# Performance work log

Measured on AMD Instinct MI355X. Metric: run time of the kernel, lower is better.

## Reference

```python
import jax, jax.numpy as jnp
import numpy as np

# ---- config constants (must match init_kwargs) ----
B, S, D, H, HD = 2, 2048, 512, 8, 64
N_BLK, L_BLK = 64, 32          # block_size, block_len (S = N_BLK*L_BLK)
R, RM = 8, 4                   # router_size, group_router_mul_factor
LN, GN, GE, GT = 8, 4, 16, 2   # moe layers, groups, group experts, topk per token
DR, DG = 128, 128
FFH = 1024
THETA = 10000.0
EPS = 1e-6

_INV_FREQ = (1.0 / THETA) ** (np.arange(0, HD, 2, dtype=np.float32) / HD)


def rmsnorm(x, w):
    return x * jax.lax.rsqrt(jnp.mean(x * x, axis=-1, keepdims=True) + EPS) * w


def rope(x):
    # x: (b, h, s, hd); y1 = x1*cos + x2*sin, y2 = -x1*sin + x2*cos (as in RotaryEmb)
    s = x.shape[2]
    freqs = jnp.outer(jnp.arange(s, dtype=jnp.float32), jnp.asarray(_INV_FREQ))[None, None]
    cos, sin = jnp.cos(freqs), jnp.sin(freqs)
    x1, x2 = jnp.split(x, 2, axis=-1)
    return jnp.concatenate([x1 * cos + x2 * sin, -x1 * sin + x2 * cos], axis=-1)


def layer(x, mask, qkv_w, o_w, up_w, down_w, n1, n2):
    b, s, d = x.shape
    xn = rmsnorm(x, n1)
    q, k, v = jnp.split(xn @ qkv_w, 3, axis=-1)
    sh = lambda t: t.reshape(b, s, H, HD).transpose(0, 2, 1, 3)  # b h s hd
    q, k, v = rope(sh(q)), rope(sh(k)), sh(v)
    scores = jnp.einsum('bhqa,bhka->bhqk', q, k) / np.sqrt(HD).astype(np.float32)
    if mask is not None:
        scores = jnp.where(mask[:, None], scores, -jnp.inf)
    p = jax.nn.softmax(scores, axis=-1)
    o = jnp.einsum('bhqk,bhka->bhqa', p, v).transpose(0, 2, 1, 3).reshape(b, s, d)
    x = x + o @ o_w
    xn2 = rmsnorm(x, n2)
    h1, h2 = jnp.split(xn2 @ up_w, 2, axis=-1)
    return x + (jax.nn.silu(h1) * h2) @ down_w


def _l2n(t, axis):
    return t / jnp.maximum(jnp.linalg.norm(t, axis=axis, keepdims=True), 1e-12)


def forward(x, doc, router_token, out_w, keys_router, keys_gate,
            enc_qkv, enc_o, enc_up, enc_down, enc_n1, enc_n2,
            rtr_qkv, rtr_o, rtr_up, rtr_down, rtr_n1, rtr_n2):
    # ---- AuxEncoder: block-causal AND same-document mask (global_attn branch) ----
    qb = jnp.arange(S) // N_BLK
    causal = qb[:, None] >= qb[None, :]                       # (S, S)
    mask = causal[None] & (doc[:, :, None] == doc[:, None, :])  # (B, S, S)
    for i in range(enc_qkv.shape[0]):
        x = layer(x, mask, enc_qkv[i], enc_o[i], enc_up[i], enc_down[i], enc_n1[i], enc_n2[i])

    # ---- AuxRouter: split into blocks, append router tokens, full attention ----
    xr = x.reshape(B * L_BLK, N_BLK, D)
    rt = jnp.broadcast_to(router_token, (B * L_BLK, R, D))
    xr = jnp.concatenate([xr, rt], axis=1)                    # (B*L, N+R, D)
    for i in range(rtr_qkv.shape[0]):
        xr = layer(xr, None, rtr_qkv[i], rtr_o[i], rtr_up[i], rtr_down[i], rtr_n1[i], rtr_n2[i])
    out = xr[:, N_BLK:] @ out_w                               # (B*L, R, DR+DG)
    xro, xgo = out[..., :DR], out[..., DR:]

    def expand(t, dd):
        # repeat '(b l) r d -> (r rm) b l d', roll(1, dim=2), flatten(1,2)
        t = t.reshape(B, L_BLK, R, dd).transpose(2, 0, 1, 3)  # (R, B, L, d)
        t = jnp.repeat(t, RM, axis=0)                          # (R*RM, B, L, d)
        t = jnp.roll(t, 1, axis=2)
        return t.reshape(R * RM, B * L_BLK, dd)

    xrr = _l2n(expand(xro, DR), -1)
    xgg = _l2n(expand(xgo, DG), -1)
    kr = _l2n(keys_router, 1)
    kg = _l2n(keys_gate, 1)
    rl = jnp.einsum('gbd,gde->gbe', xrr, kr)                  # (LN*GN, B*L, GE)
    gl = jnp.einsum('gbd,gde->gbe', xgg, kg)
    _, idx = jax.lax.top_k(rl, GT)                            # (LN*GN, B*L, GT)
    rv = jnp.take_along_axis(rl, idx, axis=-1)
    gv = jnp.take_along_axis(gl, idx, axis=-1)
    return jnp.stack([rv, gv], axis=0)                        # (2, 32, 64, 2)


def setup_inputs() -> dict:
    key = jax.random.key(0)
    ks = jax.random.split(key, 20)
    w = lambda k, shp: 0.02 * jax.random.normal(k, shp, dtype=jnp.float32)
    return {
        'x': jax.random.normal(ks[0], (B, S, D), dtype=jnp.float32),
        'doc': jnp.sort(jax.random.randint(ks[1], (B, S), 0, 4), axis=-1),
        'router_token': jax.random.normal(ks[2], (1, R, D), dtype=jnp.float32),
        'out_w': w(ks[3], (D, DR + DG)),
        'keys_router': jax.random.normal(ks[4], (LN * GN, DR, GE), dtype=jnp.float32),
        'keys_gate': jax.random.normal(ks[5], (LN * GN, DG, GE), dtype=jnp.float32),
        'enc_qkv': w(ks[6], (4, D, 3 * D)),
        'enc_o': w(ks[7], (4, D, D)),
        'enc_up': w(ks[8], (4, D, 2 * FFH)),
        'enc_down': w(ks[9], (4, FFH, D)),
        'enc_n1': jnp.ones((4, D), dtype=jnp.float32),
        'enc_n2': jnp.ones((4, D), dtype=jnp.float32),
        'rtr_qkv': w(ks[10], (2, D, 3 * D)),
        'rtr_o': w(ks[11], (2, D, D)),
        'rtr_up': w(ks[12], (2, D, 2 * FFH)),
        'rtr_down': w(ks[13], (2, FFH, D)),
        'rtr_n1': jnp.ones((2, D), dtype=jnp.float32),
        'rtr_n2': jnp.ones((2, D), dtype=jnp.float32),
    }


def reference(x, doc, router_token, out_w, keys_router, keys_gate,
              enc_qkv, enc_o, enc_up, enc_down, enc_n1, enc_n2,
              rtr_qkv, rtr_o, rtr_up, rtr_down, rtr_n1, rtr_n2):
    return forward(x, doc, router_token, out_w, keys_router, keys_gate,
                   enc_qkv, enc_o, enc_up, enc_down, enc_n1, enc_n2,
                   rtr_qkv, rtr_o, rtr_up, rtr_down, rtr_n1, rtr_n2)
```

## Files before the change

### kernel.cpp

```cpp
#include <hip/hip_runtime.h>
#include <hip/hip_bf16.h>
#include <cstdint>


typedef __attribute__((ext_vector_type(8))) short short8;
typedef __attribute__((ext_vector_type(4))) float f32x4;
typedef unsigned short ushort_t;

__device__ __forceinline__ float bf2f(unsigned short u) {
    return __uint_as_float(((unsigned)u) << 16);
}
__device__ __forceinline__ unsigned short f2bf(float f) {
    unsigned u = __float_as_uint(f);
    unsigned r = 0x7FFFu + ((u >> 16) & 1u);
    return (unsigned short)((u + r) >> 16);
}
__device__ __forceinline__ float wave_sum64(float v) {
#pragma unroll
    for (int o = 32; o; o >>= 1) v += __shfl_xor(v, o);
    return v;
}
__device__ __forceinline__ void load_lds16(const ushort_t* g, ushort_t* l) {
    __builtin_amdgcn_global_load_lds(
        (const __attribute__((address_space(1))) unsigned int*)g,
        (__attribute__((address_space(3))) unsigned int*)l, 16, 0, 0);
}

#define MFMA16(a, b, c) __builtin_amdgcn_mfma_f32_16x16x32_bf16(a, b, c, 0, 0, 0)
#define BARRIER_RAW() do { asm volatile("" ::: "memory"); \
    __builtin_amdgcn_s_barrier(); asm volatile("" ::: "memory"); } while (0)

__global__ void copy_in_kernel(const float* __restrict__ src,
                               float* __restrict__ dst, int n) {
    int i = blockIdx.x * 256 + threadIdx.x;
    if (i < n) dst[i] = src[i];
}

__global__ __launch_bounds__(256) void wsplit_kernel(const float* __restrict__ W,
        unsigned short* __restrict__ WH, unsigned short* __restrict__ WL,
        int K, int N) {
    __shared__ float tile[32][33];
    int bn = blockIdx.x * 32, bk = blockIdx.y * 32;
    int tx = threadIdx.x & 31, ty = threadIdx.x >> 5;
#pragma unroll
    for (int i = 0; i < 4; ++i)
        tile[ty + 8 * i][tx] = W[(size_t)(bk + ty + 8 * i) * N + bn + tx];
    __syncthreads();
#pragma unroll
    for (int i = 0; i < 4; ++i) {
        int n = bn + ty + 8 * i, k = bk + tx;
        float x = tile[tx][ty + 8 * i];
        unsigned short h = f2bf(x);
        unsigned short lo = f2bf(x - bf2f(h));
        WH[(size_t)n * K + k] = h;
        WL[(size_t)n * K + k] = lo;
    }
}

__global__ __launch_bounds__(256) void rmsnorm_kernel(const float* __restrict__ X,
        const float* __restrict__ W, ushort_t* __restrict__ XNH,
        ushort_t* __restrict__ XNL) {
    int t = blockIdx.x, tid = threadIdx.x;
    const float* xr = X + (size_t)t * 512;
    float v0 = xr[tid], v1 = xr[tid + 256];
    float ss = wave_sum64(v0 * v0 + v1 * v1);
    __shared__ float red[4];
    if ((tid & 63) == 0) red[tid >> 6] = ss;
    __syncthreads();
    float tot = red[0] + red[1] + red[2] + red[3];
    float scale = rsqrtf(tot * (1.0f / 512.0f) + 1e-6f);
    float a0 = v0 * scale * W[tid];
    float a1 = v1 * scale * W[tid + 256];
    unsigned short h0 = f2bf(a0), h1 = f2bf(a1);
    size_t base = (size_t)t * 512;
    XNH[base + tid]       = h0;
    XNL[base + tid]       = f2bf(a0 - bf2f(h0));
    XNH[base + tid + 256] = h1;
    XNL[base + tid + 256] = f2bf(a1 - bf2f(h1));
}

template <int BM>
__global__ __launch_bounds__(256) void gemm3(
        const ushort_t* __restrict__ AH, const ushort_t* __restrict__ AL,
        const ushort_t* __restrict__ BH, const ushort_t* __restrict__ BL,
        const float* __restrict__ Res, float* __restrict__ C,
        int M, int N, int K) {
    constexpr int MI   = BM / 32;
    constexpr int ROWS = 2 * BM + 256;
    constexpr int LPW  = ROWS / 64;
    constexpr int SS   = ROWS * 32;
    __shared__ __align__(16) ushort_t S[3][ROWS][32];
    int tid = threadIdx.x;
    int n0 = blockIdx.x * 128, m0 = blockIdx.y * BM;
    int wid = tid >> 6, lane = tid & 63;
    int wm = (wid >> 1) * (BM / 2), wn = (wid & 1) * 64;
    int col = lane & 15, quad = lane >> 4;

    const ushort_t* gsrc[LPW];
    int ldof[LPW];
#pragma unroll
    for (int j = 0; j < LPW; ++j) {
        int e = wid * LPW + j;
        int srow = e * 16 + (lane >> 2);
        const ushort_t* gp; int rin;
        if (srow < BM)                { gp = AH + (size_t)m0 * K; rin = srow; }
        else if (srow < 2 * BM)       { gp = AL + (size_t)m0 * K; rin = srow - BM; }
        else if (srow < 2 * BM + 128) { gp = BH + (size_t)n0 * K; rin = srow - 2 * BM; }
        else                          { gp = BL + (size_t)n0 * K; rin = srow - 2 * BM - 128; }
        gsrc[j] = gp + (size_t)rin * K + ((lane & 3) ^ ((lane >> 3) & 3)) * 8;
        ldof[j] = e * 512;
    }
    ushort_t* sbase = &S[0][0][0];
    auto STAGE = [&](int set, int kc) {
        ushort_t* sb = sbase + set * SS;
#pragma unroll
        for (int j = 0; j < LPW; ++j)
            load_lds16(gsrc[j] + kc * 32, sb + ldof[j]);
    };
    auto WAITK = [&]() {
        if constexpr (BM == 64) asm volatile("s_waitcnt vmcnt(6)" ::: "memory");
        else                    asm volatile("s_waitcnt vmcnt(8)" ::: "memory");
    };

    int chrd = (quad ^ ((col >> 1) & 3)) * 8;
    f32x4 acc[MI][4] = {};
    int nk = K >> 5;
    STAGE(0, 0);
    if (nk > 1) { STAGE(1, 1); WAITK(); }
    else        { asm volatile("s_waitcnt vmcnt(0)" ::: "memory"); }
    BARRIER_RAW();
    int sc = 0, sn = 1, sp = 2;
#pragma unroll 1
    for (int kc = 0; kc < nk; ++kc) {
        if (kc + 2 < nk) STAGE(sp, kc + 2);
        const ushort_t* sb = sbase + sc * SS;
        short8 afh[MI], afl[MI], bfh[4], bfl[4];
#pragma unroll
        for (int i = 0; i < MI; ++i) {
            afh[i] = *(const short8*)(sb + (size_t)(wm + i * 16 + col) * 32 + chrd);
            afl[i] = *(const short8*)(sb + (size_t)(BM + wm + i * 16 + col) * 32 + chrd);
        }
#pragma unroll
        for (int i = 0; i < 4; ++i) {
            bfh[i] = *(const short8*)(sb + (size_t)(2 * BM + wn + i * 16 + col) * 32 + chrd);
            bfl[i] = *(const short8*)(sb + (size_t)(2 * BM + 128 + wn + i * 16 + col) * 32 + chrd);
        }
#pragma unroll
        for (int mi = 0; mi < MI; ++mi)
#pragma unroll
            for (int ni = 0; ni < 4; ++ni) {
                f32x4 c = acc[mi][ni];
                c = MFMA16(afh[mi], bfh[ni], c);
                c = MFMA16(afh[mi], bfl[ni], c);
                c = MFMA16(afl[mi], bfh[ni], c);
                acc[mi][ni] = c;
            }
        if (kc + 1 < nk) {
            if (kc + 2 < nk) WAITK();
            else asm volatile("s_waitcnt vmcnt(0)" ::: "memory");
            BARRIER_RAW();
        }
        int t = sc; sc = sn; sn = sp; sp = t;
    }
#pragma unroll
    for (int mi = 0; mi < MI; ++mi)
#pragma unroll
        for (int ni = 0; ni < 4; ++ni)
#pragma unroll
            for (int r = 0; r < 4; ++r) {
                int row = m0 + wm + mi * 16 + quad * 4 + r;
                int ccol = n0 + wn + ni * 16 + col;
                size_t o = (size_t)row * N + ccol;
                float v = acc[mi][ni][r];
                if (Res) v += Res[o];
                C[o] = v;
            }
}

__global__ void rope_pack_kernel(const float* __restrict__ QKV,
        float* __restrict__ Q, ushort_t* __restrict__ KH,
        ushort_t* __restrict__ KL, int Sg, int total) {
    int idx = blockIdx.x * 256 + threadIdx.x;
    if (idx >= total) return;
    int i = idx & 31;
    int h = (idx >> 5) & 7;
    int t = idx >> 8;
    int g = t / Sg; int s = t - g * Sg;
    const float* row = QKV + (size_t)t * 1536;
    float inv = powf(10000.0f, -(float)(2 * i) / 64.0f);
    float sn, cs;
    sincosf((float)s * inv, &sn, &cs);
    size_t ob = ((size_t)(g * 8 + h) * Sg + s) * 64 + i;
    int c = h * 64 + i;
    float q1 = row[c], q2 = row[c + 32];
    Q[ob]      = q1 * cs + q2 * sn;
    Q[ob + 32] = q2 * cs - q1 * sn;
    float k1 = row[512 + c], k2 = row[512 + c + 32];
    float ka = k1 * cs + k2 * sn;
    float kb = k2 * cs - k1 * sn;
    unsigned short ha = f2bf(ka), hb = f2bf(kb);
    KH[ob]      = ha;  KL[ob]      = f2bf(ka - bf2f(ha));
    KH[ob + 32] = hb;  KL[ob + 32] = f2bf(kb - bf2f(hb));
}

__global__ __launch_bounds__(256) void vtrans_kernel(const float* __restrict__ QKV,
        ushort_t* __restrict__ VTH, ushort_t* __restrict__ VTL, int Sg) {
    __shared__ float tile[64][65];
    int chunk = blockIdx.x, gh = blockIdx.y;
    int g = gh >> 3, h = gh & 7;
    int tid = threadIdx.x;
    int sr = tid >> 2, dc = (tid & 3) * 16;
    int s = chunk * 64 + sr;
    if (s < Sg) {
        const float* src = QKV + ((size_t)g * Sg + s) * 1536 + 1024 + h * 64 + dc;
#pragma unroll
        for (int j = 0; j < 4; ++j) {
            float4 v = *(const float4*)(src + 4 * j);
            tile[sr][dc + 4 * j]     = v.x;
            tile[sr][dc + 4 * j + 1] = v.y;
            tile[sr][dc + 4 * j + 2] = v.z;
            tile[sr][dc + 4 * j + 3] = v.w;
        }
    } else {
#pragma unroll
        for (int j = 0; j < 16; ++j) tile[sr][dc + j] = 0.f;
    }
    __syncthreads();
    int dr = tid >> 2, sc = (tid & 3) * 16;
    short8 hv[2], lv[2];
#pragma unroll
    for (int half = 0; half < 2; ++half)
#pragma unroll
        for (int j = 0; j < 8; ++j) {
            float v = tile[sc + half * 8 + j][dr];
            unsigned short hb = f2bf(v);
            hv[half][j] = (short)hb;
            lv[half][j] = (short)f2bf(v - bf2f(hb));
        }
    int scol = chunk * 64 + sc;
    size_t ob = ((size_t)gh * 64 + dr) * Sg + scol;
    if (scol + 16 <= Sg) {
        *(short8*)(VTH + ob)     = hv[0];
        *(short8*)(VTH + ob + 8) = hv[1];
        *(short8*)(VTL + ob)     = lv[0];
        *(short8*)(VTL + ob + 8) = lv[1];
    } else {
#pragma unroll
        for (int j = 0; j < 16; ++j)
            if (scol + j < Sg) {
                VTH[ob + j] = (ushort_t)((j < 8) ? hv[0][j] : hv[1][j - 8]);
                VTL[ob + j] = (ushort_t)((j < 8) ? lv[0][j] : lv[1][j - 8]);
            }
    }
}

template <bool MASKED>
__global__ __launch_bounds__(256, 3) void attn3_kernel(const float* __restrict__ Q,
        const ushort_t* __restrict__ KHg, const ushort_t* __restrict__ KLg,
        const ushort_t* __restrict__ VTHg, const ushort_t* __restrict__ VTLg,
        const int* __restrict__ doc, ushort_t* __restrict__ AOH,
        ushort_t* __restrict__ AOL, int Sg) {
    __shared__ __align__(16) ushort_t Khs[64][64], Kls[64][64];
    __shared__ __align__(16) ushort_t Vts[64][64], Vtl[64][64];
    __shared__ __align__(16) ushort_t Ph[4][16][72], Pl[4][16][72];
    __shared__ int dock[64];
    int qb = (int)(gridDim.x - 1 - blockIdx.x);
    int gh = blockIdx.y, g = gh >> 3;
    int tid = threadIdx.x, wid = tid >> 6, lane = tid & 63;
    int col = lane & 15, quad = lane >> 4;

    int rL = lane >> 3, cSw = (lane & 7) ^ rL;
    const ushort_t* kb;
    const ushort_t* vb;
    ushort_t* lb;
    if (wid == 0)      { kb = KHg + (size_t)gh * Sg * 64 + cSw * 8;  vb = nullptr; lb = &Khs[0][0]; }
    else if (wid == 1) { kb = KLg + (size_t)gh * Sg * 64 + cSw * 8;  vb = nullptr; lb = &Kls[0][0]; }
    else if (wid == 2) { vb = VTHg + ((size_t)gh * 64 + rL) * Sg;    kb = nullptr; lb = &Vts[0][0]; }
    else               { vb = VTLg + ((size_t)gh * 64 + rL) * Sg;    kb = nullptr; lb = &Vtl[0][0]; }
    int sw0 = ((0 + quad) ^ (col & 7)) * 8;
    int sw1 = ((4 + quad) ^ (col & 7)) * 8;

    short8 qa[2][2];
    {
        int qrow = qb * 64 + wid * 16 + col;
        if (qrow >= Sg) qrow = Sg - 1;
        const float* Qg = Q + ((size_t)gh * Sg + qrow) * 64 + quad * 8;
#pragma unroll
        for (int kk = 0; kk < 2; ++kk) {
            float4 v0 = *(const float4*)(Qg + kk * 32);
            float4 v1 = *(const float4*)(Qg + kk * 32 + 4);
            float vv[8] = {v0.x, v0.y, v0.z, v0.w, v1.x, v1.y, v1.z, v1.w};
            short8 h, l;
#pragma unroll
            for (int e = 0; e < 8; ++e) {
                float x = vv[e] * 0.125f;
                unsigned short hb = f2bf(x);
                h[e] = (short)hb;
                l[e] = (short)f2bf(x - bf2f(hb));
            }
            qa[kk][0] = h; qa[kk][1] = l;
        }
    }
    int dqr[4]; int wq0 = 0, wq1 = 0, bq0 = 0, bq1 = 0;
    if (MASKED) {
        const int* db = doc + (size_t)g * Sg + qb * 64;
#pragma unroll
        for (int r = 0; r < 4; ++r) dqr[r] = db[wid * 16 + quad * 4 + r];
        wq0 = db[wid * 16]; wq1 = db[wid * 16 + 15];
        bq0 = db[0];        bq1 = db[63];
    }
    float m[4], l[4];
    f32x4 accO[4];
#pragma unroll
    for (int r = 0; r < 4; ++r) { m[r] = -1e30f; l[r] = 0.f; }
#pragma unroll
    for (int nd = 0; nd < 4; ++nd) accO[nd] = (f32x4){0.f, 0.f, 0.f, 0.f};

    int nkt = MASKED ? (qb + 1) : ((Sg + 63) >> 6);
    for (int kt = 0; kt < nkt; ++kt) {
        int kval = Sg - kt * 64; if (kval > 64) kval = 64;
        __syncthreads();
        if (MASKED) {
            if (tid < 64) dock[tid] = doc[(size_t)g * Sg + kt * 64 + tid];
            __syncthreads();
        }
        bool bskip = false;
        if (MASKED) bskip = (dock[63] < bq0) || (dock[0] > bq1);
        if (!bskip) {
            if (wid < 2) {
#pragma unroll
                for (int p = 0; p < 8; ++p) {
                    int sr2 = kt * 64 + p * 8 + rL;
                    if (sr2 > Sg - 1) sr2 = Sg - 1;
                    load_lds16(kb + (size_t)sr2 * 64, lb + p * 512);
                }
            } else {
                int vc = kt * 64 + cSw * 8;
                if (vc > Sg - 8) vc = Sg - 8;
#pragma unroll
                for (int p = 0; p < 8; ++p)
                    load_lds16(vb + (size_t)(p * 8) * Sg + vc, lb + p * 512);
            }
            __syncthreads();
            bool wskip = false;
            if (MASKED) wskip = (dock[kval - 1] < wq0) || (dock[0] > wq1);
            if (!wskip) {
                int dk[4];
                if (MASKED) {
#pragma unroll
                    for (int ni = 0; ni < 4; ++ni) dk[ni] = dock[ni * 16 + col];
                }
                f32x4 sc[4];
#pragma unroll
                for (int ni = 0; ni < 4; ++ni) {
                    int rb = (ni * 16 + col) * 64;
                    short8 bh0 = *(const short8*)(&Khs[0][0] + rb + sw0);
                    short8 bl0 = *(const short8*)(&Kls[0][0] + rb + sw0);
                    short8 bh1 = *(const short8*)(&Khs[0][0] + rb + sw1);
                    short8 bl1 = *(const short8*)(&Kls[0][0] + rb + sw1);
                    f32x4 c = (f32x4){0.f, 0.f, 0.f, 0.f};
                    c = MFMA16(qa[0][0], bh0, c);
                    c = MFMA16(qa[0][0], bl0, c);
                    c = MFMA16(qa[0][1], bh0, c);
                    c = MFMA16(qa[1][0], bh1, c);
                    c = MFMA16(qa[1][0], bl1, c);
                    c = MFMA16(qa[1][1], bh1, c);
                    sc[ni] = c;
                }
                float mnew[4];
#pragma unroll
                for (int r = 0; r < 4; ++r) mnew[r] = -1e30f;
#pragma unroll
                for (int ni = 0; ni < 4; ++ni)
#pragma unroll
                    for (int r = 0; r < 4; ++r) {
                        bool ok = MASKED ? (dk[ni] == dqr[r]) : (ni * 16 + col < kval);
                        float s = ok ? sc[ni][r] : -1e30f;
                        sc[ni][r] = s;
                        mnew[r] = fmaxf(mnew[r], s);
                    }
#pragma unroll
                for (int r = 0; r < 4; ++r)
#pragma unroll
                    for (int o = 1; o < 16; o <<= 1)
                        mnew[r] = fmaxf(mnew[r], __shfl_xor(mnew[r], o));
                float alpha[4], lsum[4];
#pragma unroll
                for (int r = 0; r < 4; ++r) {
                    float M = fmaxf(m[r], mnew[r]);
                    alpha[r] = __expf(m[r] - M);
                    m[r] = M;
                    lsum[r] = 0.f;
                }
#pragma unroll
                for (int ni = 0; ni < 4; ++ni)
#pragma unroll
                    for (int r = 0; r < 4; ++r) {
                        bool ok = MASKED ? (dk[ni] == dqr[r]) : (ni * 16 + col < kval);
                        float p = ok ? __expf(sc[ni][r] - m[r]) : 0.f;
                        lsum[r] += p;
                        unsigned short h = f2bf(p);
                        Ph[wid][quad * 4 + r][ni * 16 + col] = h;
                        Pl[wid][quad * 4 + r][ni * 16 + col] = f2bf(p - bf2f(h));
                    }
#pragma unroll
                for (int r = 0; r < 4; ++r) {
#pragma unroll
                    for (int o = 1; o < 16; o <<= 1)
                        lsum[r] += __shfl_xor(lsum[r], o);
                    l[r] = l[r] * alpha[r] + lsum[r];
                }
#pragma unroll
                for (int nd = 0; nd < 4; ++nd)
#pragma unroll
                    for (int r = 0; r < 4; ++r) accO[nd][r] *= alpha[r];
#pragma unroll
                for (int kk = 0; kk < 2; ++kk) {
                    short8 pah = *(const short8*)&Ph[wid][col][kk * 32 + quad * 8];
                    short8 pal = *(const short8*)&Pl[wid][col][kk * 32 + quad * 8];
                    int sw = kk ? sw1 : sw0;
#pragma unroll
                    for (int nd = 0; nd < 4; ++nd) {
                        int rb = (nd * 16 + col) * 64;
                        short8 vbh = *(const short8*)(&Vts[0][0] + rb + sw);
                        short8 vbl = *(const short8*)(&Vtl[0][0] + rb + sw);
                        f32x4 c = accO[nd];
                        c = MFMA16(pah, vbh, c);
                        c = MFMA16(pah, vbl, c);
                        c = MFMA16(pal, vbh, c);
                        accO[nd] = c;
                    }
                }
            }
        }
    }
#pragma unroll
    for (int r = 0; r < 4; ++r) {
        int qrow = qb * 64 + wid * 16 + quad * 4 + r;
        if (qrow < Sg) {
            float inv = 1.0f / l[r];
            size_t base = ((size_t)g * Sg + qrow) * 512 + (gh & 7) * 64;
#pragma unroll
            for (int nd = 0; nd < 4; ++nd) {
                float val = accO[nd][r] * inv;
                unsigned short h = f2bf(val);
                AOH[base + nd * 16 + col] = h;
                AOL[base + nd * 16 + col] = f2bf(val - bf2f(h));
            }
        }
    }
}

__global__ void silu_mul_kernel(const float* __restrict__ H,
        ushort_t* __restrict__ MIDH, ushort_t* __restrict__ MIDL, int total) {
    int idx = blockIdx.x * 256 + threadIdx.x;
    if (idx >= total) return;
    int t = idx >> 10, j = idx & 1023;
    float a = H[(size_t)t * 2048 + j];
    float b = H[(size_t)t * 2048 + 1024 + j];
    float r = (a / (1.0f + __expf(-a))) * b;
    unsigned short h = f2bf(r);
    MIDH[idx] = h;
    MIDL[idx] = f2bf(r - bf2f(h));
}

__global__ void router_build_kernel(const float* __restrict__ X,
        const float* __restrict__ RT, float* __restrict__ X2, int total) {
    int idx = blockIdx.x * 256 + threadIdx.x;
    if (idx >= total) return;
    int d = idx & 511;
    int p = (idx >> 9) % 72;
    int g2 = idx / (72 * 512);
    X2[idx] = (p < 64) ? X[((size_t)g2 * 64 + p) * 512 + d]
                       : RT[(p - 64) * 512 + d];
}

__global__ void gather_rows_kernel(const float* __restrict__ X2,
        ushort_t* __restrict__ RRH, ushort_t* __restrict__ RRL, int total) {
    int idx = blockIdx.x * 256 + threadIdx.x;
    if (idx >= total) return;
    int d = idx & 511;
    int row = idx >> 9;
    int g2 = row >> 3, rr = row & 7;
    float v = X2[((size_t)(g2 * 72 + 64 + rr)) * 512 + d];
    unsigned short h = f2bf(v);
    RRH[idx] = h;
    RRL[idx] = f2bf(v - bf2f(h));
}

__global__ __launch_bounds__(64) void norm_half_kernel(const float* __restrict__ IN,
        float* __restrict__ OUT) {
    int b = blockIdx.x; int lane = threadIdx.x;
    size_t base = (size_t)(b >> 1) * 256 + (size_t)(b & 1) * 128;
    float v0 = IN[base + lane], v1 = IN[base + 64 + lane];
    float ss = wave_sum64(v0 * v0 + v1 * v1);
    float sc = 1.0f / fmaxf(sqrtf(ss), 1e-12f);
    OUT[base + lane]      = v0 * sc;
    OUT[base + 64 + lane] = v1 * sc;
}

__global__ __launch_bounds__(64) void norm_keys_kernel(const float* __restrict__ Kin,
        float* __restrict__ Kout) {
    int b = blockIdx.x; int lane = threadIdx.x;
    int g = b >> 4, e = b & 15;
    size_t base = (size_t)g * 2048 + e;
    float v0 = Kin[base + (size_t)lane * 16];
    float v1 = Kin[base + (size_t)(lane + 64) * 16];
    float ss = wave_sum64(v0 * v0 + v1 * v1);
    float sc = 1.0f / fmaxf(sqrtf(ss), 1e-12f);
    Kout[base + (size_t)lane * 16]        = v0 * sc;
    Kout[base + (size_t)(lane + 64) * 16] = v1 * sc;
}

__global__ __launch_bounds__(64) void logits_top2_kernel(const float* __restrict__ OUTN,
        const float* __restrict__ KRN, const float* __restrict__ KGN,
        float* __restrict__ out) {
    int blk = blockIdx.x;
    int g = blk >> 6, bcol = blk & 63;
    int b = bcol >> 5, l = bcol & 31;
    int lsrc = (l + 31) & 31;
    int r = g >> 2;
    int row = (b * 32 + lsrc) * 8 + r;
    const float* rvec = OUTN + (size_t)row * 256;
    __shared__ float sc[32];
    int lane = threadIdx.x;
    if (lane < 32) {
        int e = lane & 15;
        const float* kb = ((lane < 16) ? KRN : KGN) + (size_t)g * 2048 + e;
        const float* xv = (lane < 16) ? rvec : (rvec + 128);
        float s = 0.f;
#pragma unroll 8
        for (int d = 0; d < 128; ++d) s = fmaf(xv[d], kb[(size_t)d * 16], s);
        sc[lane] = s;
    }
    __syncthreads();
    if (lane == 0) {
        float bv = -1e30f, sv = -1e30f; int bi = 0, si = 0;
#pragma unroll
        for (int e = 0; e < 16; ++e) {
            float v = sc[e];
            if (v > bv) { sv = bv; si = bi; bv = v; bi = e; }
            else if (v > sv) { sv = v; si = e; }
        }
        size_t base = (size_t)g * 128 + (size_t)bcol * 2;
        out[base]            = bv;
        out[base + 1]        = sv;
        out[4096 + base]     = sc[16 + bi];
        out[4096 + base + 1] = sc[16 + si];
    }
}

static void run_layer(float* X, float* BIG, float* Qb,
                      ushort_t* KHb, ushort_t* KLb, ushort_t* VTHb, ushort_t* VTLb,
                      ushort_t* XNH, ushort_t* XNL, ushort_t* AOH, ushort_t* AOL,
                      ushort_t* MIDH, ushort_t* MIDL,
                      const unsigned short* WH, const unsigned short* WL,
                      const float* n1, const float* n2,
                      const int* doc, int G, int Sg, hipStream_t stream) {
    const size_t oQKV = 0, oO = 786432, oUP = 1048576, oDN = 2097152;
    int T = G * Sg;
    rmsnorm_kernel<<<T, 256, 0, stream>>>(X, n1, XNH, XNL);
    gemm3<64><<<dim3(12, T / 64), 256, 0, stream>>>(XNH, XNL, WH + oQKV, WL + oQKV, nullptr, BIG, T, 1536, 512);
    int rp = T * 256;
    rope_pack_kernel<<<(rp + 255) / 256, 256, 0, stream>>>(BIG, Qb, KHb, KLb, Sg, rp);
    int qblocks = (Sg + 63) >> 6;
    vtrans_kernel<<<dim3(qblocks, G * 8), 256, 0, stream>>>(BIG, VTHb, VTLb, Sg);
    if (doc)
        attn3_kernel<true><<<dim3(qblocks, G * 8), 256, 0, stream>>>(Qb, KHb, KLb, VTHb, VTLb, doc, AOH, AOL, Sg);
    else
        attn3_kernel<false><<<dim3(qblocks, G * 8), 256, 0, stream>>>(Qb, KHb, KLb, VTHb, VTLb, nullptr, AOH, AOL, Sg);
    gemm3<64><<<dim3(4, T / 64), 256, 0, stream>>>(AOH, AOL, WH + oO, WL + oO, X, X, T, 512, 512);
    rmsnorm_kernel<<<T, 256, 0, stream>>>(X, n2, XNH, XNL);
    gemm3<64><<<dim3(16, T / 64), 256, 0, stream>>>(XNH, XNL, WH + oUP, WL + oUP, nullptr, BIG, T, 2048, 512);
    silu_mul_kernel<<<(T * 1024 + 255) / 256, 256, 0, stream>>>(BIG, MIDH, MIDL, T * 1024);
    gemm3<64><<<dim3(4, T / 64), 256, 0, stream>>>(MIDH, MIDL, WH + oDN, WL + oDN, X, X, T, 512, 1024);
}

static void split_layer(const float* qkv, const float* o, const float* up, const float* dn,
                        unsigned short* WH, unsigned short* WL, hipStream_t stream) {
    const size_t oQKV = 0, oO = 786432, oUP = 1048576, oDN = 2097152;
    wsplit_kernel<<<dim3(48, 16), 256, 0, stream>>>(qkv, WH + oQKV, WL + oQKV, 512, 1536);
    wsplit_kernel<<<dim3(16, 16), 256, 0, stream>>>(o,   WH + oO,   WL + oO,   512, 512);
    wsplit_kernel<<<dim3(64, 16), 256, 0, stream>>>(up,  WH + oUP,  WL + oUP,  512, 2048);
    wsplit_kernel<<<dim3(16, 32), 256, 0, stream>>>(dn,  WH + oDN,  WL + oDN,  1024, 512);
}

extern "C" void kernel_launch(void* const* d_in, const int* in_sizes, int n_in,
                              void* d_out, int out_size, void* d_ws, size_t ws_size,
                              hipStream_t stream) {
    const float* x_in    = (const float*)d_in[0];
    const int*   doc     = (const int*)d_in[1];
    const float* rt      = (const float*)d_in[2];
    const float* out_w   = (const float*)d_in[3];
    const float* k_rt    = (const float*)d_in[4];
    const float* k_gt    = (const float*)d_in[5];
    const float* enc_qkv = (const float*)d_in[6];
    const float* enc_o   = (const float*)d_in[7];
    const float* enc_up  = (const float*)d_in[8];
    const float* enc_dn  = (const float*)d_in[9];
    const float* enc_n1  = (const float*)d_in[10];
    const float* enc_n2  = (const float*)d_in[11];
    const float* rtr_qkv = (const float*)d_in[12];
    const float* rtr_o   = (const float*)d_in[13];
    const float* rtr_up  = (const float*)d_in[14];
    const float* rtr_dn  = (const float*)d_in[15];
    const float* rtr_n1  = (const float*)d_in[16];
    const float* rtr_n2  = (const float*)d_in[17];

    float* ws = (float*)d_ws;
    size_t off = 0;
    auto alloc = [&](size_t n) { float* p = ws + off; off += n; return p; };
    float* X    = alloc(4608UL * 512);
    float* X2   = alloc(4608UL * 512);
    float* BIG  = alloc(4608UL * 2048);
    float* Qb   = alloc(4608UL * 512);
    ushort_t* KHb  = (ushort_t*)alloc(1179648UL);
    ushort_t* KLb  = (ushort_t*)alloc(1179648UL);
    ushort_t* VTHb = (ushort_t*)alloc(1179648UL);
    ushort_t* VTLb = (ushort_t*)alloc(1179648UL);
    unsigned short* WH = (unsigned short*)(ws + off);
    unsigned short* WL = WH + 2621440UL;
    off += 2621440UL;
    ushort_t* XNH = (ushort_t*)Qb;
    ushort_t* XNL = XNH + 4608UL * 512;
    ushort_t* MIDH = (ushort_t*)Qb;
    ushort_t* MIDL = (ushort_t*)KHb;
    ushort_t* AOH = (ushort_t*)BIG;
    ushort_t* AOL = AOH + 4608UL * 512;
    ushort_t* RRH = (ushort_t*)X;
    ushort_t* RRL = RRH + 262144;
    float* OUTM = X + 262144;
    float* OUTN = X + 393216;
    float* KRN  = X + 524288;
    float* KGN  = X + 589824;
    (void)ws_size; (void)in_sizes; (void)n_in; (void)out_size;

    copy_in_kernel<<<(2097152 + 255) / 256, 256, 0, stream>>>(x_in, X, 2097152);

    for (int i = 0; i < 4; ++i) {
        split_layer(enc_qkv + (size_t)i * 512 * 1536,
                    enc_o   + (size_t)i * 512 * 512,
                    enc_up  + (size_t)i * 512 * 2048,
                    enc_dn  + (size_t)i * 1024 * 512, WH, WL, stream);
        run_layer(X, BIG, Qb, KHb, KLb, VTHb, VTLb, XNH, XNL, AOH, AOL, MIDH, MIDL,
                  WH, WL, enc_n1 + (size_t)i * 512, enc_n2 + (size_t)i * 512,
                  doc, 2, 2048, stream);
    }

    int rb_total = 64 * 72 * 512;
    router_build_kernel<<<(rb_total + 255) / 256, 256, 0, stream>>>(X, rt, X2, rb_total);

    for (int i = 0; i < 2; ++i) {
        split_layer(rtr_qkv + (size_t)i * 512 * 1536,
                    rtr_o   + (size_t)i * 512 * 512,
                    rtr_up  + (size_t)i * 512 * 2048,
                    rtr_dn  + (size_t)i * 1024 * 512, WH, WL, stream);
        run_layer(X2, BIG, Qb, KHb, KLb, VTHb, VTLb, XNH, XNL, AOH, AOL, MIDH, MIDL,
                  WH, WL, rtr_n1 + (size_t)i * 512, rtr_n2 + (size_t)i * 512,
                  nullptr, 64, 72, stream);
    }

    gather_rows_kernel<<<(512 * 512) / 256, 256, 0, stream>>>(X2, RRH, RRL, 512 * 512);
    wsplit_kernel<<<dim3(8, 16), 256, 0, stream>>>(out_w, WH, WL, 512, 256);
    gemm3<64><<<dim3(2, 8), 256, 0, stream>>>(RRH, RRL, WH, WL, nullptr, OUTM, 512, 256, 512);

    norm_half_kernel<<<1024, 64, 0, stream>>>(OUTM, OUTN);
    norm_keys_kernel<<<512, 64, 0, stream>>>(k_rt, KRN);
    norm_keys_kernel<<<512, 64, 0, stream>>>(k_gt, KGN);
    logits_top2_kernel<<<2048, 64, 0, stream>>>(OUTN, KRN, KGN, (float*)d_out);
}
```

Baseline: 1.371 ms.

## Fuse up-projection GEMM with SiLU-gating and switch GEMM to double buffering

Adds a dedicated up-projection GEMM that computes the gate and value halves together per tile and applies SiLU*mul in the epilogue, writing the bf16 hi/lo split directly. This removes the separate silu_mul kernel and the fp32 round trip of the 2048-wide intermediate. The generic gemm3 also drops from triple to double LDS buffering with a full vmcnt(0) wait, which reduces LDS use but exposes more load latency. MID buffers are relocated into BIG so they no longer alias XNH (Qb).

```diff
diff --git a/kernel.cpp b/kernel.cpp
--- a/kernel.cpp
+++ b/kernel.cpp
@@ -29,6 +29,7 @@
 #define MFMA16(a, b, c) __builtin_amdgcn_mfma_f32_16x16x32_bf16(a, b, c, 0, 0, 0)
 #define BARRIER_RAW() do { asm volatile("" ::: "memory"); \
     __builtin_amdgcn_s_barrier(); asm volatile("" ::: "memory"); } while (0)
+#define VMCNT0() asm volatile("s_waitcnt vmcnt(0)" ::: "memory")
 
 __global__ void copy_in_kernel(const float* __restrict__ src,
                                float* __restrict__ dst, int n) {
@@ -89,7 +90,7 @@
     constexpr int ROWS = 2 * BM + 256;
     constexpr int LPW  = ROWS / 64;
     constexpr int SS   = ROWS * 32;
-    __shared__ __align__(16) ushort_t S[3][ROWS][32];
+    __shared__ __align__(16) ushort_t S[2][ROWS][32];
     int tid = threadIdx.x;
     int n0 = blockIdx.x * 128, m0 = blockIdx.y * BM;
     int wid = tid >> 6, lane = tid & 63;
@@ -117,23 +118,18 @@
         for (int j = 0; j < LPW; ++j)
             load_lds16(gsrc[j] + kc * 32, sb + ldof[j]);
     };
-    auto WAITK = [&]() {
-        if constexpr (BM == 64) asm volatile("s_waitcnt vmcnt(6)" ::: "memory");
-        else                    asm volatile("s_waitcnt vmcnt(8)" ::: "memory");
-    };
 
     int chrd = (quad ^ ((col >> 1) & 3)) * 8;
     f32x4 acc[MI][4] = {};
     int nk = K >> 5;
     STAGE(0, 0);
-    if (nk > 1) { STAGE(1, 1); WAITK(); }
-    else        { asm volatile("s_waitcnt vmcnt(0)" ::: "memory"); }
+    VMCNT0();
     BARRIER_RAW();
-    int sc = 0, sn = 1, sp = 2;
+    int cur = 0;
 #pragma unroll 1
     for (int kc = 0; kc < nk; ++kc) {
-        if (kc + 2 < nk) STAGE(sp, kc + 2);
-        const ushort_t* sb = sbase + sc * SS;
+        if (kc + 1 < nk) STAGE(cur ^ 1, kc + 1);
+        const ushort_t* sb = sbase + cur * SS;
         short8 afh[MI], afl[MI], bfh[4], bfl[4];
 #pragma unroll
         for (int i = 0; i < MI; ++i) {
@@ -156,11 +152,10 @@
                 acc[mi][ni] = c;
             }
         if (kc + 1 < nk) {
-            if (kc + 2 < nk) WAITK();
-            else asm volatile("s_waitcnt vmcnt(0)" ::: "memory");
+            VMCNT0();
             BARRIER_RAW();
-        }
-        int t = sc; sc = sn; sn = sp; sp = t;
+            cur ^= 1;
+        }
     }
 #pragma unroll
     for (int mi = 0; mi < MI; ++mi)
@@ -174,6 +169,106 @@
                 float v = acc[mi][ni][r];
                 if (Res) v += Res[o];
                 C[o] = v;
+            }
+}
+
+__global__ __launch_bounds__(256) void gemm_up_silu(
+        const ushort_t* __restrict__ AH, const ushort_t* __restrict__ AL,
+        const ushort_t* __restrict__ BH, const ushort_t* __restrict__ BL,
+        ushort_t* __restrict__ MIDH, ushort_t* __restrict__ MIDL, int K) {
+    constexpr int ROWS = 640;
+    constexpr int LPW  = 10;
+    constexpr int SS   = ROWS * 32;
+    __shared__ __align__(16) ushort_t S[2][ROWS][32];
+    int tid = threadIdx.x;
+    int n0 = blockIdx.x * 128, m0 = blockIdx.y * 64;
+    int wid = tid >> 6, lane = tid & 63;
+    int wm = (wid >> 1) * 32, wn = (wid & 1) * 64;
+    int col = lane & 15, quad = lane >> 4;
+
+    const ushort_t* gsrc[LPW];
+    int ldof[LPW];
+#pragma unroll
+    for (int j = 0; j < LPW; ++j) {
+        int e = wid * LPW + j;
+        int srow = e * 16 + (lane >> 2);
+        const ushort_t* gp; int rin;
+        if (srow < 64)       { gp = AH; rin = m0 + srow; }
+        else if (srow < 128) { gp = AL; rin = m0 + srow - 64; }
+        else if (srow < 256) { gp = BH; rin = n0 + srow - 128; }
+        else if (srow < 384) { gp = BL; rin = n0 + srow - 256; }
+        else if (srow < 512) { gp = BH; rin = 1024 + n0 + srow - 384; }
+        else                 { gp = BL; rin = 1024 + n0 + srow - 512; }
+        gsrc[j] = gp + (size_t)rin * K + ((lane & 3) ^ ((lane >> 3) & 3)) * 8;
+        ldof[j] = e * 512;
+    }
+    ushort_t* sbase = &S[0][0][0];
+    auto STAGE = [&](int set, int kc) {
+        ushort_t* sb = sbase + set * SS;
+#pragma unroll
+        for (int j = 0; j < LPW; ++j)
+            load_lds16(gsrc[j] + kc * 32, sb + ldof[j]);
+    };
+
+    int chrd = (quad ^ ((col >> 1) & 3)) * 8;
+    f32x4 a1[2][4] = {}, a2[2][4] = {};
+    int nk = K >> 5;
+    STAGE(0, 0);
+    VMCNT0();
+    BARRIER_RAW();
+    int cur = 0;
+#pragma unroll 1
+    for (int kc = 0; kc < nk; ++kc) {
+        if (kc + 1 < nk) STAGE(cur ^ 1, kc + 1);
+        const ushort_t* sb = sbase + cur * SS;
+        short8 afh[2], afl[2], b1h[4], b1l[4], b2h[4], b2l[4];
+#pragma unroll
+        for (int i = 0; i < 2; ++i) {
+            afh[i] = *(const short8*)(sb + (size_t)(wm + i * 16 + col) * 32 + chrd);
+            afl[i] = *(const short8*)(sb + (size_t)(64 + wm + i * 16 + col) * 32 + chrd);
+        }
+#pragma unroll
+        for (int i = 0; i < 4; ++i) {
+            b1h[i] = *(const short8*)(sb + (size_t)(128 + wn + i * 16 + col) * 32 + chrd);
+            b1l[i] = *(const short8*)(sb + (size_t)(256 + wn + i * 16 + col) * 32 + chrd);
+            b2h[i] = *(const short8*)(sb + (size_t)(384 + wn + i * 16 + col) * 32 + chrd);
+            b2l[i] = *(const short8*)(sb + (size_t)(512 + wn + i * 16 + col) * 32 + chrd);
+        }
+#pragma unroll
+        for (int mi = 0; mi < 2; ++mi)
+#pragma unroll
+            for (int ni = 0; ni < 4; ++ni) {
+                f32x4 c = a1[mi][ni];
+                c = MFMA16(afh[mi], b1h[ni], c);
+                c = MFMA16(afh[mi], b1l[ni], c);
+                c = MFMA16(afl[mi], b1h[ni], c);
+                a1[mi][ni] = c;
+                f32x4 d = a2[mi][ni];
+                d = MFMA16(afh[mi], b2h[ni], d);
+                d = MFMA16(afh[mi], b2l[ni], d);
+                d = MFMA16(afl[mi], b2h[ni], d);
+                a2[mi][ni] = d;
+            }
+        if (kc + 1 < nk) {
+            VMCNT0();
+            BARRIER_RAW();
+            cur ^= 1;
+        }
+    }
+#pragma unroll
+    for (int mi = 0; mi < 2; ++mi)
+#pragma unroll
+        for (int ni = 0; ni < 4; ++ni)
+#pragma unroll
+            for (int r = 0; r < 4; ++r) {
+                int row = m0 + wm + mi * 16 + quad * 4 + r;
+                int ccol = n0 + wn + ni * 16 + col;
+                float v1 = a1[mi][ni][r], v2 = a2[mi][ni][r];
+                float rr = (v1 / (1.0f + __expf(-v1))) * v2;
+                unsigned short h = f2bf(rr);
+                size_t o = (size_t)row * 1024 + ccol;
+                MIDH[o] = h;
+                MIDL[o] = f2bf(rr - bf2f(h));
             }
 }
 
@@ -451,19 +546,6 @@
     }
 }
 
-__global__ void silu_mul_kernel(const float* __restrict__ H,
-        ushort_t* __restrict__ MIDH, ushort_t* __restrict__ MIDL, int total) {
-    int idx = blockIdx.x * 256 + threadIdx.x;
-    if (idx >= total) return;
-    int t = idx >> 10, j = idx & 1023;
-    float a = H[(size_t)t * 2048 + j];
-    float b = H[(size_t)t * 2048 + 1024 + j];
-    float r = (a / (1.0f + __expf(-a))) * b;
-    unsigned short h = f2bf(r);
-    MIDH[idx] = h;
-    MIDL[idx] = f2bf(r - bf2f(h));
-}
-
 __global__ void router_build_kernel(const float* __restrict__ X,
         const float* __restrict__ RT, float* __restrict__ X2, int total) {
     int idx = blockIdx.x * 256 + threadIdx.x;
@@ -571,8 +653,7 @@
         attn3_kernel<false><<<dim3(qblocks, G * 8), 256, 0, stream>>>(Qb, KHb, KLb, VTHb, VTLb, nullptr, AOH, AOL, Sg);
     gemm3<64><<<dim3(4, T / 64), 256, 0, stream>>>(AOH, AOL, WH + oO, WL + oO, X, X, T, 512, 512);
     rmsnorm_kernel<<<T, 256, 0, stream>>>(X, n2, XNH, XNL);
-    gemm3<64><<<dim3(16, T / 64), 256, 0, stream>>>(XNH, XNL, WH + oUP, WL + oUP, nullptr, BIG, T, 2048, 512);
-    silu_mul_kernel<<<(T * 1024 + 255) / 256, 256, 0, stream>>>(BIG, MIDH, MIDL, T * 1024);
+    gemm_up_silu<<<dim3(8, T / 64), 256, 0, stream>>>(XNH, XNL, WH + oUP, WL + oUP, MIDH, MIDL, 512);
     gemm3<64><<<dim3(4, T / 64), 256, 0, stream>>>(MIDH, MIDL, WH + oDN, WL + oDN, X, X, T, 512, 1024);
 }
 
@@ -623,10 +704,10 @@
     off += 2621440UL;
     ushort_t* XNH = (ushort_t*)Qb;
     ushort_t* XNL = XNH + 4608UL * 512;
-    ushort_t* MIDH = (ushort_t*)Qb;
-    ushort_t* MIDL = (ushort_t*)KHb;
     ushort_t* AOH = (ushort_t*)BIG;
     ushort_t* AOL = AOH + 4608UL * 512;
+    ushort_t* MIDH = (ushort_t*)BIG;
+    ushort_t* MIDL = MIDH + 4608UL * 1024;
     ushort_t* RRH = (ushort_t*)X;
     ushort_t* RRL = RRH + 262144;
     float* OUTM = X + 262144;
```

Result: faster. 1.300 ms (-5.1%).
